# Kernel tuning notes

Hardware: AMD Instinct MI355X
Metric: run time of the kernel (lower is better)

The kernel has to match this reference:

```python
import jax, jax.numpy as jnp
import numpy as np

B, S = 32, 2048
D = 128      # embedding_dim
H = 256      # hidden_dim
K = 512      # codebook_size
RECON_COEF, COMMIT_COEF, VQ_COEF = 1.0, 0.15, 0.05


def _conv1d(x, w, b):
    # x: [B, Cin, S], w: [Cout, Cin, 3], 'SAME' padding (padding=1, k=3)
    y = jax.lax.conv_general_dilated(x, w, window_strides=(1,), padding='SAME',
                                     dimension_numbers=('NCH', 'OIH', 'NCH'))
    return y + b[None, :, None]


def _lrelu(x):
    return jnp.where(x >= 0, x, 0.2 * x)


def setup_inputs() -> dict:
    key = jax.random.key(0)
    ks = jax.random.split(key, 14)

    def w(k, shape, fan_in):
        bound = 1.0 / np.sqrt(fan_in)
        return jax.random.uniform(k, shape, jnp.float32, -bound, bound)

    return {
        'x': jax.random.normal(ks[0], (B, S), jnp.float32),
        'codebook': jax.random.normal(ks[1], (K, D), jnp.float32),
        'ew1': w(ks[2], (H, 1, 3), 1 * 3),  'eb1': w(ks[3], (H,), 1 * 3),
        'ew2': w(ks[4], (H, H, 3), H * 3),  'eb2': w(ks[5], (H,), H * 3),
        'ew3': w(ks[6], (D, H, 3), H * 3),  'eb3': w(ks[7], (D,), H * 3),
        'dw1': w(ks[8], (H, D, 3), D * 3),  'db1': w(ks[9], (H,), D * 3),
        'dw2': w(ks[10], (H, H, 3), H * 3), 'db2': w(ks[11], (H,), H * 3),
        'dw3': w(ks[12], (1, H, 3), H * 3), 'db3': w(ks[13], (1,), H * 3),
    }


def reference(x, codebook, ew1, eb1, ew2, eb2, ew3, eb3, dw1, db1, dw2, db2, dw3, db3):
    # ---- encode ----
    h = x[:, None, :]                                  # [B,1,S]
    h = _lrelu(_conv1d(h, ew1, eb1))
    h = _lrelu(_conv1d(h, ew2, eb2))
    z = _conv1d(h, ew3, eb3)                           # [B,D,S]

    # ---- vector quantize (eval mode: no EMA update) ----
    zt = jnp.transpose(z, (0, 2, 1))                   # [B,S,D]
    z_flat = zt.reshape(-1, D)                         # [B*S,D]
    # squared distances: |z|^2 + |c|^2 - 2 z c^T
    d = (jnp.sum(z_flat ** 2, axis=1, keepdims=True)
         + jnp.sum(codebook ** 2, axis=1)
         - 2.0 * z_flat @ codebook.T)                  # [B*S,K]
    idx = jnp.argmin(d, axis=1)                        # [B*S]
    z_q = codebook[idx].reshape(zt.shape)              # [B,S,D] (== one-hot @ codebook)

    vq_loss = jnp.mean((jax.lax.stop_gradient(zt) - z_q) ** 2) * VQ_COEF
    commitment_loss = jnp.mean((zt - jax.lax.stop_gradient(z_q)) ** 2) * COMMIT_COEF
    indices = idx.reshape(B, S)

    # ---- decode ----
    h = jnp.transpose(z_q, (0, 2, 1))                  # [B,D,S]
    h = _lrelu(_conv1d(h, dw1, db1))
    h = _lrelu(_conv1d(h, dw2, db2))
    x_recon = _conv1d(h, dw3, db3)[:, 0, :]            # [B,S]

    recon_loss = jnp.mean((x - x_recon) ** 2) * RECON_COEF
    loss = recon_loss + vq_loss + commitment_loss
    return x_recon, indices, loss, recon_loss, vq_loss, commitment_loss
```

## Files before the change

### kernel.cpp

```cpp
#include <hip/hip_runtime.h>
#include <float.h>

#define S_LEN 2048
#define BATCH 32
#define HCH   256
#define DCH   128
#define KCODES 512

typedef float  f32x4  __attribute__((ext_vector_type(4)));
typedef short  bf16x8 __attribute__((ext_vector_type(8)));
typedef short  short8 __attribute__((ext_vector_type(8)));

__device__ __forceinline__ float lrelu_f(float v) { return v >= 0.f ? v : 0.2f * v; }

__device__ __forceinline__ short f2bf(float f) {
    unsigned u = __float_as_uint(f);
    u = u + 0x7fffu + ((u >> 16) & 1u);
    return (short)(u >> 16);
}
__device__ __forceinline__ float bf2f(unsigned short u) {
    return __uint_as_float(((unsigned)u) << 16);
}

__device__ __forceinline__ void async_copy16(short* lds, const short* g) {
    __builtin_amdgcn_global_load_lds(
        (const __attribute__((address_space(1))) unsigned int*)g,
        (__attribute__((address_space(3))) unsigned int*)lds,
        16, 0, 0);
}

__global__ void prep_cb_split_kernel(const float* __restrict__ cb,
                                     short* __restrict__ cb_hi, short* __restrict__ cb_lo,
                                     float* __restrict__ cnorm) {
    int k = blockIdx.x * 256 + threadIdx.x;
    if (k < KCODES) {
        float s = 0.f;
        for (int d = 0; d < DCH; ++d) {
            float v = cb[k * DCH + d];
            s += v * v;
            short hi = f2bf(v);
            short lo = f2bf(v - bf2f((unsigned short)hi));
            cb_hi[k * DCH + d] = hi;
            cb_lo[k * DCH + d] = lo;
        }
        cnorm[k] = s;
    }
}

__global__ void prep_w_split_kernel(const float* __restrict__ Wsrc,
                                    short* __restrict__ Wh, short* __restrict__ Wl,
                                    int Cout, int Cin) {
    int i = blockIdx.x * 256 + threadIdx.x;
    int total = 3 * Cout * Cin;
    if (i < total) {
        int t = i / (Cout * Cin);
        int rem = i - t * Cout * Cin;
        int co = rem / Cin;
        int ci = rem - co * Cin;
        float v = Wsrc[(co * Cin + ci) * 3 + t];
        short hi = f2bf(v);
        Wh[i] = hi;
        Wl[i] = f2bf(v - bf2f((unsigned short)hi));
    }
}

__global__ void prep_wdec_kernel(const float* __restrict__ Wsrc, short* __restrict__ Wdst,
                                 int Cin) {
    int i = blockIdx.x * 256 + threadIdx.x;
    int total = 3 * 256 * Cin;
    if (i < total) {
        int t = i / (256 * Cin);
        int rem = i - t * 256 * Cin;
        int co = rem / Cin;
        int ci = rem - co * Cin;
        Wdst[i] = f2bf(Wsrc[(co * Cin + ci) * 3 + t]);
    }
}

__global__ void prep_w3t_kernel(const float* __restrict__ w3, float* __restrict__ w3t) {
    int i = blockIdx.x * 256 + threadIdx.x;
    if (i < 768) {
        int t = i / 256, ci = i - t * 256;
        w3t[i] = w3[ci * 3 + t];
    }
}

__global__ __launch_bounds__(256) void enc_conv1_cl_kernel(
        const float* __restrict__ x, short* __restrict__ h_hi, short* __restrict__ h_lo,
        const float* __restrict__ w, const float* __restrict__ bias) {
    __shared__ float ws[HCH * 3];
    __shared__ float bs[HCH];
    int tid = threadIdx.x;
    for (int i = tid; i < HCH * 3; i += 256) ws[i] = w[i];
    for (int i = tid; i < HCH; i += 256) bs[i] = bias[i];
    __syncthreads();
    int b = blockIdx.y;
    int s = blockIdx.x * 32 + (tid >> 3);
    int cch = tid & 7;
    const float* xb = x + (size_t)b * S_LEN;
    float xm = (s > 0) ? xb[s - 1] : 0.f;
    float x0 = xb[s];
    float xp = (s < S_LEN - 1) ? xb[s + 1] : 0.f;
    size_t base = ((size_t)(b * S_LEN + s)) * HCH + cch * 32;
#pragma unroll
    for (int cc = 0; cc < 4; ++cc) {
        short8 oh, ol;
#pragma unroll
        for (int e = 0; e < 8; ++e) {
            int co = cch * 32 + cc * 8 + e;
            float v = ws[co * 3 + 0] * xm + ws[co * 3 + 1] * x0 + ws[co * 3 + 2] * xp + bs[co];
            v = lrelu_f(v);
            short hi = f2bf(v);
            oh[e] = hi;
            ol[e] = f2bf(v - bf2f((unsigned short)hi));
        }
        *(short8*)(h_hi + base + cc * 8) = oh;
        *(short8*)(h_lo + base + cc * 8) = ol;
    }
}

__global__ __launch_bounds__(256, 3) void conv_mfma_split(
        const short* __restrict__ in_hi, const short* __restrict__ in_lo,
        short* __restrict__ out_hi, short* __restrict__ out_lo,
        const short* __restrict__ wt_hi, const short* __restrict__ wt_lo,
        const float* __restrict__ bias, int Cin, int Cout, int do_lrelu) {
    __shared__ short smem[16640];

    const int tid  = threadIdx.x;
    const int lane = tid & 63;
    const int w    = tid >> 6;
    const int m    = lane & 15;
    const int q    = lane >> 4;
    const int sOff = (w & 1) * 64;
    const int cOff = (w >> 1) * 64;
    const int b    = blockIdx.z;
    const int s0   = blockIdx.x * 128;
    const int co0  = blockIdx.y * 128;

    f32x4 acc[4][4];
    f32x4 zero4 = {0.f, 0.f, 0.f, 0.f};
#pragma unroll
    for (int i = 0; i < 4; ++i)
#pragma unroll
        for (int j = 0; j < 4; ++j) acc[i][j] = zero4;

    const short* inhb = in_hi + (size_t)b * S_LEN * Cin;
    const short* inlb = in_lo + (size_t)b * S_LEN * Cin;
    const char* XhB = (const char*)smem;
    const char* XlB = XhB + 1040 * 16;

    for (int ci0 = 0; ci0 < Cin; ci0 += 64) {
        __syncthreads();

        if (s0 == 0 && tid < 16) {
            short8 z = {0, 0, 0, 0, 0, 0, 0, 0};
            int buf = tid >> 3, slot = tid & 7;
            *(short8*)(smem + (size_t)(buf * 1040 + slot) * 8) = z;
        }
        if (s0 == S_LEN - 128 && tid < 16) {
            short8 z = {0, 0, 0, 0, 0, 0, 0, 0};
            int buf = tid >> 3, slot = tid & 7;
            *(short8*)(smem + (size_t)(buf * 1040 + 129 * 8 + slot) * 8) = z;
        }

        for (int c = tid; c < 2080; c += 256) {
            int base_c = c - lane;
            int buf  = (c >= 1040) ? 1 : 0;
            int cc   = c - buf * 1040;
            int r    = cc >> 3;
            int slot = cc & 7;
            int gch  = slot ^ (r & 7);
            int s    = s0 - 1 + r;
            short* ldsb = smem + (size_t)base_c * 8;
            const short* gp = (buf ? inlb : inhb) + (size_t)s * Cin + ci0 + gch * 8;
            if (s >= 0 && s < S_LEN) async_copy16(ldsb, gp);
        }
        __syncthreads();

#pragma unroll 1
        for (int ks = 0; ks < 2; ++ks) {
#pragma unroll
            for (int t = 0; t < 3; ++t) {
                bf16x8 ah[4], al[4], bh[4], bl[4];
#pragma unroll
                for (int i = 0; i < 4; ++i) {
                    int row = sOff + i * 16 + m + t;
                    int off = row * 128 + (((ks * 4 + q) ^ (row & 7)) << 4);
                    ah[i] = *(const bf16x8*)(XhB + off);
                    al[i] = *(const bf16x8*)(XlB + off);
                }
#pragma unroll
                for (int j = 0; j < 4; ++j) {
                    size_t woff = ((size_t)(t * Cout + co0 + cOff + j * 16 + m)) * Cin
                                  + ci0 + ks * 32 + q * 8;
                    bh[j] = *(const bf16x8*)(wt_hi + woff);
                    bl[j] = *(const bf16x8*)(wt_lo + woff);
                }
#pragma unroll
                for (int i = 0; i < 4; ++i)
#pragma unroll
                    for (int j = 0; j < 4; ++j) {
                        acc[i][j] = __builtin_amdgcn_mfma_f32_16x16x32_bf16(ah[i], bh[j], acc[i][j], 0, 0, 0);
                        acc[i][j] = __builtin_amdgcn_mfma_f32_16x16x32_bf16(ah[i], bl[j], acc[i][j], 0, 0, 0);
                        acc[i][j] = __builtin_amdgcn_mfma_f32_16x16x32_bf16(al[i], bh[j], acc[i][j], 0, 0, 0);
                    }
            }
        }
    }

    __syncthreads();

    short* ob = smem + w * 4096;
#pragma unroll
    for (int pass = 0; pass < 2; ++pass) {
#pragma unroll
        for (int j = 0; j < 4; ++j) {
            float bv = bias[co0 + cOff + j * 16 + m];
#pragma unroll
            for (int i = 0; i < 4; ++i)
#pragma unroll
                for (int r = 0; r < 4; ++r) {
                    float val = acc[i][j][r] + bv;
                    if (do_lrelu) val = lrelu_f(val);
                    short hi = f2bf(val);
                    short v = pass ? f2bf(val - bf2f((unsigned short)hi)) : hi;
                    ob[(i * 16 + q * 4 + r) * 64 + j * 16 + m] = v;
                }
        }
        short* outp = pass ? out_lo : out_hi;
#pragma unroll
        for (int itr = 0; itr < 8; ++itr) {
            int row = itr * 8 + (lane >> 3);
            int ch  = lane & 7;
            short8 v = *(const short8*)(ob + row * 64 + ch * 8);
            size_t goff = ((size_t)(b * S_LEN + s0 + sOff + row)) * Cout
                          + co0 + cOff + ch * 8;
            *(short8*)(outp + goff) = v;
        }
    }
}

__global__ __launch_bounds__(256) void vq_mfma_kernel(
        const short* __restrict__ z_hi, const short* __restrict__ z_lo,
        const short* __restrict__ cb_hi, const short* __restrict__ cb_lo,
        const float* __restrict__ cnorm, const float* __restrict__ cb,
        int* __restrict__ idx_out, float* __restrict__ idx_f_out,
        short* __restrict__ zq, float* __restrict__ acc_vq) {
    __shared__ short smem[2 * 64 * 136];
    __shared__ float redv[64][4];
    __shared__ int   redi[64][4];
    __shared__ int   idxs[64];
    __shared__ float wsum2[4];
    short* Zh = smem;
    short* Zl = smem + 64 * 136;

    const int tid = threadIdx.x;
    const int lane = tid & 63;
    const int w = tid >> 6;
    const int m = lane & 15;
    const int q = lane >> 4;
    const int n0 = blockIdx.x * 64;

    for (int c = tid; c < 2048; c += 256) {
        int buf = c >> 10;
        int rem = c & 1023;
        int r = rem >> 4, part = rem & 15;
        size_t goff = (size_t)(n0 + r) * DCH + part * 8;
        float4 v = buf ? *(const float4*)(z_lo + goff) : *(const float4*)(z_hi + goff);
        *(float4*)((buf ? Zl : Zh) + r * 136 + part * 8) = v;
    }
    __syncthreads();

    float best[4][4];
    int besti[4][4];
#pragma unroll
    for (int i = 0; i < 4; ++i)
#pragma unroll
        for (int r = 0; r < 4; ++r) { best[i][r] = FLT_MAX; besti[i][r] = 0; }

    for (int k0 = 0; k0 < KCODES; k0 += 256) {
        f32x4 acc[4][4];
        f32x4 zero4 = {0.f, 0.f, 0.f, 0.f};
#pragma unroll
        for (int i = 0; i < 4; ++i)
#pragma unroll
            for (int j = 0; j < 4; ++j) acc[i][j] = zero4;

#pragma unroll
        for (int d0 = 0; d0 < DCH; d0 += 32) {
            bf16x8 ah[4], al[4], bh[4], bl[4];
#pragma unroll
            for (int i = 0; i < 4; ++i) {
                int row = i * 16 + m;
                ah[i] = *(const bf16x8*)(Zh + row * 136 + d0 + q * 8);
                al[i] = *(const bf16x8*)(Zl + row * 136 + d0 + q * 8);
            }
#pragma unroll
            for (int j = 0; j < 4; ++j) {
                size_t coff = (size_t)(k0 + w * 64 + j * 16 + m) * DCH + d0 + q * 8;
                bh[j] = *(const bf16x8*)(cb_hi + coff);
                bl[j] = *(const bf16x8*)(cb_lo + coff);
            }
#pragma unroll
            for (int i = 0; i < 4; ++i)
#pragma unroll
                for (int j = 0; j < 4; ++j) {
                    acc[i][j] = __builtin_amdgcn_mfma_f32_16x16x32_bf16(ah[i], bh[j], acc[i][j], 0, 0, 0);
                    acc[i][j] = __builtin_amdgcn_mfma_f32_16x16x32_bf16(ah[i], bl[j], acc[i][j], 0, 0, 0);
                    acc[i][j] = __builtin_amdgcn_mfma_f32_16x16x32_bf16(al[i], bh[j], acc[i][j], 0, 0, 0);
                }
        }
#pragma unroll
        for (int j = 0; j < 4; ++j) {
            int k = k0 + w * 64 + j * 16 + m;
            float cn = cnorm[k];
#pragma unroll
            for (int i = 0; i < 4; ++i)
#pragma unroll
                for (int r = 0; r < 4; ++r) {
                    float dv = cn - 2.f * acc[i][j][r];
                    if (dv < best[i][r]) { best[i][r] = dv; besti[i][r] = k; }
                }
        }
    }

#pragma unroll
    for (int mask = 1; mask < 16; mask <<= 1) {
#pragma unroll
        for (int i = 0; i < 4; ++i)
#pragma unroll
            for (int r = 0; r < 4; ++r) {
                float ov = __shfl_xor(best[i][r], mask);
                int oi = __shfl_xor(besti[i][r], mask);
                if (ov < best[i][r] || (ov == best[i][r] && oi < besti[i][r])) {
                    best[i][r] = ov; besti[i][r] = oi;
                }
            }
    }
    if (m == 0) {
#pragma unroll
        for (int i = 0; i < 4; ++i)
#pragma unroll
            for (int r = 0; r < 4; ++r) {
                int srow = i * 16 + q * 4 + r;
                redv[srow][w] = best[i][r];
                redi[srow][w] = besti[i][r];
            }
    }
    __syncthreads();
    if (tid < 64) {
        float bv = redv[tid][0];
        int bi = redi[tid][0];
#pragma unroll
        for (int w2 = 1; w2 < 4; ++w2) {
            float v = redv[tid][w2];
            int ii = redi[tid][w2];
            if (v < bv || (v == bv && ii < bi)) { bv = v; bi = ii; }
        }
        int n = n0 + tid;
        idx_out[n] = bi;
        idx_f_out[n] = (float)bi;
        idxs[tid] = bi;
    }
    __syncthreads();

    {
        int r = tid >> 2;
        int dpart = tid & 3;
        int k = idxs[r];
        const float* src = cb + (size_t)k * DCH + dpart * 32;
        const short* zh = Zh + r * 136 + dpart * 32;
        const short* zl = Zl + r * 136 + dpart * 32;
        size_t zoff = (size_t)(n0 + r) * DCH + dpart * 32;
        float sum = 0.f;
#pragma unroll
        for (int h = 0; h < 4; ++h) {
            float4 f0 = *(const float4*)(src + h * 8);
            float4 f1 = *(const float4*)(src + h * 8 + 4);
            bf16x8 vh = *(const bf16x8*)(zh + h * 8);
            bf16x8 vl = *(const bf16x8*)(zl + h * 8);
            float qv[8] = {f0.x, f0.y, f0.z, f0.w, f1.x, f1.y, f1.z, f1.w};
            short8 o;
#pragma unroll
            for (int e = 0; e < 8; ++e) {
                o[e] = f2bf(qv[e]);
                float zv = bf2f((unsigned short)vh[e]) + bf2f((unsigned short)vl[e]);
                float df = zv - qv[e];
                sum += df * df;
            }
            *(short8*)(zq + zoff + h * 8) = o;
        }
        for (int off = 32; off > 0; off >>= 1) sum += __shfl_down(sum, off);
        if (lane == 0) wsum2[w] = sum;
    }
    __syncthreads();
    if (tid == 0) atomicAdd(acc_vq, wsum2[0] + wsum2[1] + wsum2[2] + wsum2[3]);
}

__global__ __launch_bounds__(256, 3) void conv_mfma_cl(
        const short* __restrict__ in, short* __restrict__ out,
        const short* __restrict__ wt, const float* __restrict__ bias,
        int Cin) {
    __shared__ short smem[16384];

    const int tid  = threadIdx.x;
    const int lane = tid & 63;
    const int w    = tid >> 6;
    const int m    = lane & 15;
    const int q    = lane >> 4;
    const int sOff = (w & 1) * 64;
    const int cOff = (w >> 1) * 64;
    const int b    = blockIdx.z;
    const int s0   = blockIdx.x * 128;
    const int co0  = blockIdx.y * 128;

    f32x4 acc[4][4];
    f32x4 zero4 = {0.f, 0.f, 0.f, 0.f};
#pragma unroll
    for (int i = 0; i < 4; ++i)
#pragma unroll
        for (int j = 0; j < 4; ++j) acc[i][j] = zero4;

    const short* inb = in + (size_t)b * S_LEN * Cin;
    const char* XB = (const char*)smem;

    for (int ci0 = 0; ci0 < Cin; ci0 += 64) {
        __syncthreads();

        if (s0 == 0 && tid < 8) {
            short8 z = {0, 0, 0, 0, 0, 0, 0, 0};
            *(short8*)(smem + (size_t)tid * 8) = z;
        }
        if (s0 == S_LEN - 128 && tid < 8) {
            short8 z = {0, 0, 0, 0, 0, 0, 0, 0};
            *(short8*)(smem + (size_t)(129 * 8 + tid) * 8) = z;
        }

        for (int c = tid; c < 1040; c += 256) {
            int base_c = c - lane;
            int r    = c >> 3;
            int slot = c & 7;
            int gch  = slot ^ (r & 7);
            int s    = s0 - 1 + r;
            short* ldsb = smem + (size_t)base_c * 8;
            const short* gp = inb + (size_t)s * Cin + ci0 + gch * 8;
            if (s >= 0 && s < S_LEN) async_copy16(ldsb, gp);
        }
        __syncthreads();

#pragma unroll 1
        for (int ks = 0; ks < 2; ++ks) {
#pragma unroll
            for (int t = 0; t < 3; ++t) {
                bf16x8 a[4], bb[4];
#pragma unroll
                for (int i = 0; i < 4; ++i) {
                    int row = sOff + i * 16 + m + t;
                    int off = row * 128 + (((ks * 4 + q) ^ (row & 7)) << 4);
                    a[i] = *(const bf16x8*)(XB + off);
                }
#pragma unroll
                for (int j = 0; j < 4; ++j) {
                    size_t woff = ((size_t)(t * 256 + co0 + cOff + j * 16 + m)) * Cin
                                  + ci0 + ks * 32 + q * 8;
                    bb[j] = *(const bf16x8*)(wt + woff);
                }
#pragma unroll
                for (int i = 0; i < 4; ++i)
#pragma unroll
                    for (int j = 0; j < 4; ++j)
                        acc[i][j] = __builtin_amdgcn_mfma_f32_16x16x32_bf16(
                            a[i], bb[j], acc[i][j], 0, 0, 0);
            }
        }
    }

    __syncthreads();

    short* ob = smem + w * 4096;
#pragma unroll
    for (int j = 0; j < 4; ++j) {
        float bv = bias[co0 + cOff + j * 16 + m];
#pragma unroll
        for (int i = 0; i < 4; ++i)
#pragma unroll
            for (int r = 0; r < 4; ++r) {
                float val = acc[i][j][r] + bv;
                val = lrelu_f(val);
                ob[(i * 16 + q * 4 + r) * 64 + j * 16 + m] = f2bf(val);
            }
    }
#pragma unroll
    for (int itr = 0; itr < 8; ++itr) {
        int row = itr * 8 + (lane >> 3);
        int ch  = lane & 7;
        short8 v = *(const short8*)(ob + row * 64 + ch * 8);
        size_t goff = ((size_t)(b * S_LEN + s0 + sOff + row)) * 256
                      + co0 + cOff + ch * 8;
        *(short8*)(out + goff) = v;
    }
}

__global__ __launch_bounds__(256) void dec_conv3_tiled_kernel(
        const short* __restrict__ h, const float* __restrict__ w3t,
        const float* __restrict__ b3, const float* __restrict__ x,
        float* __restrict__ xr, float* __restrict__ acc_recon) {
    __shared__ short Zs[66 * 264];
    __shared__ float ws[3 * 256];
    __shared__ float wsum[4];
    int tid = threadIdx.x;
    int b = blockIdx.y;
    int s0 = blockIdx.x * 64;
    const short* hb = h + (size_t)b * S_LEN * HCH;
    for (int i = tid; i < 768; i += 256) ws[i] = w3t[i];
    for (int c = tid; c < 2112; c += 256) {
        int r = c >> 5, part = c & 31;
        int g = s0 - 1 + r;
        short8 v = {0, 0, 0, 0, 0, 0, 0, 0};
        if (g >= 0 && g < S_LEN)
            v = *(const short8*)(hb + (size_t)g * HCH + part * 8);
        *(short8*)(Zs + r * 264 + part * 8) = v;
    }
    __syncthreads();

    int quarter = tid & 3;
    int sl = tid >> 2;
    float a0 = 0.f, a1 = 0.f, a2 = 0.f, a3 = 0.f;
#pragma unroll
    for (int t = 0; t < 3; ++t) {
        const short* zrow = Zs + (sl + t) * 264 + quarter * 64;
        const float* wrow = ws + t * 256 + quarter * 64;
#pragma unroll
        for (int c = 0; c < 8; ++c) {
            bf16x8 v = *(const bf16x8*)(zrow + c * 8);
            float4 w0 = *(const float4*)(wrow + c * 8);
            float4 w1 = *(const float4*)(wrow + c * 8 + 4);
            a0 = fmaf(w0.x, bf2f((unsigned short)v[0]), a0);
            a1 = fmaf(w0.y, bf2f((unsigned short)v[1]), a1);
            a2 = fmaf(w0.z, bf2f((unsigned short)v[2]), a2);
            a3 = fmaf(w0.w, bf2f((unsigned short)v[3]), a3);
            a0 = fmaf(w1.x, bf2f((unsigned short)v[4]), a0);
            a1 = fmaf(w1.y, bf2f((unsigned short)v[5]), a1);
            a2 = fmaf(w1.z, bf2f((unsigned short)v[6]), a2);
            a3 = fmaf(w1.w, bf2f((unsigned short)v[7]), a3);
        }
    }
    float acc = (a0 + a1) + (a2 + a3);
    acc += __shfl_xor(acc, 1);
    acc += __shfl_xor(acc, 2);
    float df2 = 0.f;
    if (quarter == 0) {
        int s = s0 + sl;
        float tot = acc + b3[0];
        xr[b * S_LEN + s] = tot;
        float df = x[b * S_LEN + s] - tot;
        df2 = df * df;
    }
    for (int off = 32; off > 0; off >>= 1) df2 += __shfl_down(df2, off);
    int lane = tid & 63, wv = tid >> 6;
    if (lane == 0) wsum[wv] = df2;
    __syncthreads();
    if (tid == 0) atomicAdd(acc_recon, wsum[0] + wsum[1] + wsum[2] + wsum[3]);
}

__global__ void finalize_kernel(const float* __restrict__ accs, float* __restrict__ out) {
    if (threadIdx.x == 0) {
        float vqm = accs[0] / ((float)BATCH * S_LEN * DCH);
        float rm  = accs[1] / ((float)BATCH * S_LEN);
        float vq_loss = vqm * 0.05f;
        float commit  = vqm * 0.15f;
        float recon   = rm * 1.0f;
        out[0] = recon + vq_loss + commit;
        out[1] = recon;
        out[2] = vq_loss;
        out[3] = commit;
    }
}

extern "C" void kernel_launch(void* const* d_in, const int* in_sizes, int n_in,
                              void* d_out, int out_size, void* d_ws, size_t ws_size,
                              hipStream_t stream) {
    const float* x    = (const float*)d_in[0];
    const float* cb   = (const float*)d_in[1];
    const float* ew1  = (const float*)d_in[2];
    const float* eb1  = (const float*)d_in[3];
    const float* ew2  = (const float*)d_in[4];
    const float* eb2  = (const float*)d_in[5];
    const float* ew3  = (const float*)d_in[6];
    const float* eb3  = (const float*)d_in[7];
    const float* dw1  = (const float*)d_in[8];
    const float* db1  = (const float*)d_in[9];
    const float* dw2  = (const float*)d_in[10];
    const float* db2  = (const float*)d_in[11];
    const float* dw3  = (const float*)d_in[12];
    const float* db3  = (const float*)d_in[13];

    float* out = (float*)d_out;
    float* xr    = out;
    float* idx_f = out + BATCH * S_LEN;
    float* loss_out = out + 2 * BATCH * S_LEN;

    const size_t NH = (size_t)BATCH * S_LEN * HCH;
    const size_t ND = (size_t)BATCH * S_LEN * DCH;

    short* sp = (short*)d_ws;
    short* h1_hi = sp;
    short* h1_lo = sp + NH;
    short* z_hi  = sp;
    short* z_lo  = sp + ND;
    short* h1d_bf = sp;
    short* h2_hi = sp + 2 * NH;
    short* h2_lo = sp + 3 * NH;
    short* zq_bf = sp + 2 * NH;
    short* h2d_bf = sp + 3 * NH;
    short* sm = sp + 4 * NH;
    short* cb_hi = sm; sm += KCODES * DCH;
    short* cb_lo = sm; sm += KCODES * DCH;
    short* w2_hi = sm; sm += 3 * HCH * HCH;
    short* w2_lo = sm; sm += 3 * HCH * HCH;
    short* w3_hi = sm; sm += 3 * DCH * HCH;
    short* w3_lo = sm; sm += 3 * DCH * HCH;
    short* wbf_d1 = sm; sm += 3 * 256 * DCH;
    short* wbf_d2 = sm; sm += 3 * 256 * HCH;
    float* cnorm = (float*)sm;
    int* idxb = (int*)(cnorm + KCODES);
    float* w3t = (float*)(idxb + BATCH * S_LEN);
    float* accs = w3t + 768;

    hipMemsetAsync(accs, 0, 2 * sizeof(float), stream);

    prep_cb_split_kernel<<<2, 256, 0, stream>>>(cb, cb_hi, cb_lo, cnorm);
    prep_w_split_kernel<<<(3 * HCH * HCH + 255) / 256, 256, 0, stream>>>(ew2, w2_hi, w2_lo, HCH, HCH);
    prep_w_split_kernel<<<(3 * DCH * HCH + 255) / 256, 256, 0, stream>>>(ew3, w3_hi, w3_lo, DCH, HCH);
    prep_wdec_kernel<<<(3 * 256 * DCH + 255) / 256, 256, 0, stream>>>(dw1, wbf_d1, DCH);
    prep_wdec_kernel<<<(3 * 256 * HCH + 255) / 256, 256, 0, stream>>>(dw2, wbf_d2, HCH);
    prep_w3t_kernel<<<3, 256, 0, stream>>>(dw3, w3t);

    enc_conv1_cl_kernel<<<dim3(S_LEN / 32, BATCH), 256, 0, stream>>>(x, h1_hi, h1_lo, ew1, eb1);
    conv_mfma_split<<<dim3(S_LEN / 128, HCH / 128, BATCH), 256, 0, stream>>>(
        h1_hi, h1_lo, h2_hi, h2_lo, w2_hi, w2_lo, eb2, HCH, HCH, 1);
    conv_mfma_split<<<dim3(S_LEN / 128, DCH / 128, BATCH), 256, 0, stream>>>(
        h2_hi, h2_lo, z_hi, z_lo, w3_hi, w3_lo, eb3, HCH, DCH, 0);

    vq_mfma_kernel<<<(BATCH * S_LEN) / 64, 256, 0, stream>>>(
        z_hi, z_lo, cb_hi, cb_lo, cnorm, cb, idxb, idx_f, zq_bf, accs);

    conv_mfma_cl<<<dim3(S_LEN / 128, 2, BATCH), 256, 0, stream>>>(
        zq_bf, h1d_bf, wbf_d1, db1, DCH);
    conv_mfma_cl<<<dim3(S_LEN / 128, 2, BATCH), 256, 0, stream>>>(
        h1d_bf, h2d_bf, wbf_d2, db2, HCH);
    dec_conv3_tiled_kernel<<<dim3(S_LEN / 64, BATCH), 256, 0, stream>>>(
        h2d_bf, w3t, db3, x, xr, accs + 1);

    finalize_kernel<<<1, 64, 0, stream>>>(accs, loss_out);
}
```

Baseline: 506.1 us.

## Double-buffer LDS input staging in the conv MFMA kernels

Both conv kernels now prefetch the next channel chunk into a second LDS buffer with async copies while MFMAs run on the current one, replacing the load-sync-compute-sync pattern. The split-precision kernel halves its chunk to 32 channels so the two hi/lo buffers fit in the same LDS footprint, and uses a 4-slot swizzle instead of an 8-slot one. The goal is to hide global-to-LDS latency behind compute. The cost is more loop iterations and barriers in the split kernel, and slightly more LDS in the plain kernel, which may affect occupancy.

```diff
diff --git a/kernel.cpp b/kernel.cpp
--- a/kernel.cpp
+++ b/kernel.cpp
@@ -146,69 +146,74 @@
 
     const short* inhb = in_hi + (size_t)b * S_LEN * Cin;
     const short* inlb = in_lo + (size_t)b * S_LEN * Cin;
-    const char* XhB = (const char*)smem;
-    const char* XlB = XhB + 1040 * 16;
-
-    for (int ci0 = 0; ci0 < Cin; ci0 += 64) {
+
+    if (s0 == 0 && tid < 16) {
+        short8 z = {0, 0, 0, 0, 0, 0, 0, 0};
+        int buf = tid >> 3, sl = tid & 7;
+        int ch = (sl < 4) ? sl : (520 + sl - 4);
+        *(short8*)(smem + buf * 8320 + ch * 8) = z;
+    }
+    if (s0 == S_LEN - 128 && tid < 16) {
+        short8 z = {0, 0, 0, 0, 0, 0, 0, 0};
+        int buf = tid >> 3, sl = tid & 7;
+        int ch = (sl < 4) ? (129 * 4 + sl) : (520 + 129 * 4 + sl - 4);
+        *(short8*)(smem + buf * 8320 + ch * 8) = z;
+    }
+
+    auto STAGE = [&](int bufSel, int ci0) {
+        for (int c = tid; c < 1040; c += 256) {
+            int base_c = c - lane;
+            int half = (c >= 520) ? 1 : 0;
+            int cc   = c - half * 520;
+            int r    = cc >> 2;
+            int slot = cc & 3;
+            int gch  = slot ^ (r & 3);
+            int s    = s0 - 1 + r;
+            short* ldsb = smem + bufSel * 8320 + (size_t)base_c * 8;
+            const short* gp = (half ? inlb : inhb) + (size_t)s * Cin + ci0 + gch * 8;
+            if (s >= 0 && s < S_LEN) async_copy16(ldsb, gp);
+        }
+    };
+
+    STAGE(0, 0);
+    __syncthreads();
+
+    const int nsteps = Cin >> 5;
+#pragma unroll 1
+    for (int step = 0; step < nsteps; ++step) {
+        const int cur = step & 1;
+        if (step + 1 < nsteps) STAGE(cur ^ 1, (step + 1) << 5);
+        const char* XhB = (const char*)(smem + cur * 8320);
+        const char* XlB = XhB + 520 * 16;
+        const int ci0 = step << 5;
+#pragma unroll
+        for (int t = 0; t < 3; ++t) {
+            bf16x8 ah[4], al[4], bh[4], bl[4];
+#pragma unroll
+            for (int i = 0; i < 4; ++i) {
+                int row = sOff + i * 16 + m + t;
+                int off = row * 64 + ((q ^ (row & 3)) << 4);
+                ah[i] = *(const bf16x8*)(XhB + off);
+                al[i] = *(const bf16x8*)(XlB + off);
+            }
+#pragma unroll
+            for (int j = 0; j < 4; ++j) {
+                size_t woff = ((size_t)(t * Cout + co0 + cOff + j * 16 + m)) * Cin
+                              + ci0 + q * 8;
+                bh[j] = *(const bf16x8*)(wt_hi + woff);
+                bl[j] = *(const bf16x8*)(wt_lo + woff);
+            }
+#pragma unroll
+            for (int i = 0; i < 4; ++i)
+#pragma unroll
+                for (int j = 0; j < 4; ++j) {
+                    acc[i][j] = __builtin_amdgcn_mfma_f32_16x16x32_bf16(ah[i], bh[j], acc[i][j], 0, 0, 0);
+                    acc[i][j] = __builtin_amdgcn_mfma_f32_16x16x32_bf16(ah[i], bl[j], acc[i][j], 0, 0, 0);
+                    acc[i][j] = __builtin_amdgcn_mfma_f32_16x16x32_bf16(al[i], bh[j], acc[i][j], 0, 0, 0);
+                }
+        }
         __syncthreads();
-
-        if (s0 == 0 && tid < 16) {
-            short8 z = {0, 0, 0, 0, 0, 0, 0, 0};
-            int buf = tid >> 3, slot = tid & 7;
-            *(short8*)(smem + (size_t)(buf * 1040 + slot) * 8) = z;
-        }
-        if (s0 == S_LEN - 128 && tid < 16) {
-            short8 z = {0, 0, 0, 0, 0, 0, 0, 0};
-            int buf = tid >> 3, slot = tid & 7;
-            *(short8*)(smem + (size_t)(buf * 1040 + 129 * 8 + slot) * 8) = z;
-        }
-
-        for (int c = tid; c < 2080; c += 256) {
-            int base_c = c - lane;
-            int buf  = (c >= 1040) ? 1 : 0;
-            int cc   = c - buf * 1040;
-            int r    = cc >> 3;
-            int slot = cc & 7;
-            int gch  = slot ^ (r & 7);
-            int s    = s0 - 1 + r;
-            short* ldsb = smem + (size_t)base_c * 8;
-            const short* gp = (buf ? inlb : inhb) + (size_t)s * Cin + ci0 + gch * 8;
-            if (s >= 0 && s < S_LEN) async_copy16(ldsb, gp);
-        }
-        __syncthreads();
-
-#pragma unroll 1
-        for (int ks = 0; ks < 2; ++ks) {
-#pragma unroll
-            for (int t = 0; t < 3; ++t) {
-                bf16x8 ah[4], al[4], bh[4], bl[4];
-#pragma unroll
-                for (int i = 0; i < 4; ++i) {
-                    int row = sOff + i * 16 + m + t;
-                    int off = row * 128 + (((ks * 4 + q) ^ (row & 7)) << 4);
-                    ah[i] = *(const bf16x8*)(XhB + off);
-                    al[i] = *(const bf16x8*)(XlB + off);
-                }
-#pragma unroll
-                for (int j = 0; j < 4; ++j) {
-                    size_t woff = ((size_t)(t * Cout + co0 + cOff + j * 16 + m)) * Cin
-                                  + ci0 + ks * 32 + q * 8;
-                    bh[j] = *(const bf16x8*)(wt_hi + woff);
-                    bl[j] = *(const bf16x8*)(wt_lo + woff);
-                }
-#pragma unroll
-                for (int i = 0; i < 4; ++i)
-#pragma unroll
-                    for (int j = 0; j < 4; ++j) {
-                        acc[i][j] = __builtin_amdgcn_mfma_f32_16x16x32_bf16(ah[i], bh[j], acc[i][j], 0, 0, 0);
-                        acc[i][j] = __builtin_amdgcn_mfma_f32_16x16x32_bf16(ah[i], bl[j], acc[i][j], 0, 0, 0);
-                        acc[i][j] = __builtin_amdgcn_mfma_f32_16x16x32_bf16(al[i], bh[j], acc[i][j], 0, 0, 0);
-                    }
-            }
-        }
-    }
-
-    __syncthreads();
+    }
 
     short* ob = smem + w * 4096;
 #pragma unroll
@@ -401,7 +406,7 @@
         const short* __restrict__ in, short* __restrict__ out,
         const short* __restrict__ wt, const float* __restrict__ bias,
         int Cin) {
-    __shared__ short smem[16384];
+    __shared__ short smem[16640];
 
     const int tid  = threadIdx.x;
     const int lane = tid & 63;
@@ -422,32 +427,41 @@
         for (int j = 0; j < 4; ++j) acc[i][j] = zero4;
 
     const short* inb = in + (size_t)b * S_LEN * Cin;
-    const char* XB = (const char*)smem;
-
-    for (int ci0 = 0; ci0 < Cin; ci0 += 64) {
-        __syncthreads();
-
-        if (s0 == 0 && tid < 8) {
-            short8 z = {0, 0, 0, 0, 0, 0, 0, 0};
-            *(short8*)(smem + (size_t)tid * 8) = z;
-        }
-        if (s0 == S_LEN - 128 && tid < 8) {
-            short8 z = {0, 0, 0, 0, 0, 0, 0, 0};
-            *(short8*)(smem + (size_t)(129 * 8 + tid) * 8) = z;
-        }
-
+
+    if (s0 == 0 && tid < 16) {
+        short8 z = {0, 0, 0, 0, 0, 0, 0, 0};
+        int buf = tid >> 3, sl = tid & 7;
+        *(short8*)(smem + buf * 8320 + sl * 8) = z;
+    }
+    if (s0 == S_LEN - 128 && tid < 16) {
+        short8 z = {0, 0, 0, 0, 0, 0, 0, 0};
+        int buf = tid >> 3, sl = tid & 7;
+        *(short8*)(smem + buf * 8320 + (129 * 8 + sl) * 8) = z;
+    }
+
+    auto STAGE = [&](int bufSel, int ci0) {
         for (int c = tid; c < 1040; c += 256) {
             int base_c = c - lane;
             int r    = c >> 3;
             int slot = c & 7;
             int gch  = slot ^ (r & 7);
             int s    = s0 - 1 + r;
-            short* ldsb = smem + (size_t)base_c * 8;
+            short* ldsb = smem + bufSel * 8320 + (size_t)base_c * 8;
             const short* gp = inb + (size_t)s * Cin + ci0 + gch * 8;
             if (s >= 0 && s < S_LEN) async_copy16(ldsb, gp);
         }
-        __syncthreads();
-
+    };
+
+    STAGE(0, 0);
+    __syncthreads();
+
+    const int nsteps = Cin >> 6;
+#pragma unroll 1
+    for (int step = 0; step < nsteps; ++step) {
+        const int cur = step & 1;
+        if (step + 1 < nsteps) STAGE(cur ^ 1, (step + 1) << 6);
+        const char* XB = (const char*)(smem + cur * 8320);
+        const int ci0 = step << 6;
 #pragma unroll 1
         for (int ks = 0; ks < 2; ++ks) {
 #pragma unroll
@@ -473,9 +487,8 @@
                             a[i], bb[j], acc[i][j], 0, 0, 0);
             }
         }
-    }
-
-    __syncthreads();
+        __syncthreads();
+    }
 
     short* ob = smem + w * 4096;
 #pragma unroll
```

Result: no change. 509.7 us (+0.7%).
